# Kernel optimization log

Measured on AMD Instinct MI355X. Metric: run time of the kernel, lower is better.

## Reference

```python
import jax, jax.numpy as jnp
import numpy as np

EPS = 1e-12  # torch F.normalize default eps


def _l2_normalize(t):
    n = jnp.linalg.norm(t, axis=-1, keepdims=True)
    return t / jnp.maximum(n, EPS)


def _block(x, W, alpha):
    # x: [B,H,N,D]; W: [D,D] (torch Linear weight, applied as x @ W.T)
    xn = _l2_normalize(x)                                   # q_norm == k_norm (q=k=x)
    A = jnp.einsum('bhnd,bhmd->bhnm', xn, xn)               # cosine similarity [B,H,N,N]
    A = jax.nn.softmax(A / jnp.maximum(alpha, 0.01), axis=-1)
    av = jnp.einsum('bhnm,bhmd->bhnd', A, x)                # A @ v, v = x
    return jax.nn.relu(jnp.einsum('bhnd,ed->bhne', av, W) + x)


def setup_inputs() -> dict:
    key = jax.random.key(0)
    k1, k2, k3 = jax.random.split(key, 3)
    B, H, N, D = 4, 4, 4096, 64
    x = jax.random.normal(k1, (B, H, N, D), dtype=jnp.float32)
    # nn.Linear(dim, dim, bias=False) weights, kaiming-uniform-ish scale
    bound = 1.0 / np.sqrt(D)
    W1 = jax.random.uniform(k2, (D, D), dtype=jnp.float32, minval=-bound, maxval=bound)
    W2 = jax.random.uniform(k3, (D, D), dtype=jnp.float32, minval=-bound, maxval=bound)
    alpha1 = jnp.float32(1.0)
    alpha2 = jnp.float32(1.0)
    return {"x": x, "W1": W1, "W2": W2, "alpha1": alpha1, "alpha2": alpha2}


def reference(x, W1, W2, alpha1, alpha2):
    x = _block(x, W1, alpha1)
    x = _block(x, W2, alpha2)
    return x
```

## Files before the change

### kernel.cpp

```cpp
#include <hip/hip_runtime.h>

typedef unsigned short u16;
typedef unsigned int   u32;
typedef __bf16 bf16x8 __attribute__((ext_vector_type(8)));
typedef float  f32x4  __attribute__((ext_vector_type(4)));

#define BH    16
#define NSEQ  4096
#define DIM   64
#define BM    128
#define BN    64
#define LDP   72
#define LDPP  68
#define NTH   32
#define QTILES (NSEQ / BM)

#define SMEM_U16   27136
#define SK_OFF     0
#define SV_OFF     9216
#define SP_OFF     18432
#define HBUF       4608
#define WOFF       13824

__device__ __forceinline__ float bf2f(u16 u) {
    union { u32 i; float f; } v; v.i = ((u32)u) << 16; return v.f;
}
__device__ __forceinline__ u16 f2bf(float f) {
    union { float f; u32 i; } v; v.f = f;
    u32 r = v.i + 0x7fffu + ((v.i >> 16) & 1u);
    return (u16)(r >> 16);
}
__device__ __forceinline__ u16 f2bf_fast(float f) {
    union { float f; u32 i; } v; v.f = f;
    return (u16)((v.i + 0x8000u) >> 16);
}
#if __has_builtin(__builtin_amdgcn_exp2f)
__device__ __forceinline__ float exp2_raw(float x) { return __builtin_amdgcn_exp2f(x); }
#else
__device__ __forceinline__ float exp2_raw(float x) {
    float r; asm("v_exp_f32 %0, %1" : "=v"(r) : "v"(x)); return r;
}
#endif

__device__ __forceinline__ void lds_barrier() {
    asm volatile("s_waitcnt lgkmcnt(0)\n\ts_barrier" ::: "memory");
}

__global__ __launch_bounds__(256) void ContentGCN_5059471475267_prep(
    const void* __restrict__ src, int isf,
    u16* __restrict__ xn, u16* __restrict__ xT)
{
    __shared__ u16 tile[256 * 72];
    int bh = blockIdx.x >> 4, nt = blockIdx.x & 15, tid = threadIdx.x;
    size_t base = ((size_t)bh * NSEQ + nt * 256 + tid) * DIM;

    float v[64];
    if (isf) {
        const float4* g = (const float4*)((const float*)src + base);
#pragma unroll
        for (int i = 0; i < 16; i++) {
            float4 t4 = g[i];
            v[4*i] = t4.x; v[4*i+1] = t4.y; v[4*i+2] = t4.z; v[4*i+3] = t4.w;
        }
    } else {
        alignas(16) u16 tmp[64];
        const uint4* g = (const uint4*)((const u16*)src + base);
#pragma unroll
        for (int i = 0; i < 8; i++) ((uint4*)tmp)[i] = g[i];
#pragma unroll
        for (int d = 0; d < 64; d++) v[d] = bf2f(tmp[d]);
    }

    float ss = 0.f;
#pragma unroll
    for (int d = 0; d < 64; d++) ss += v[d] * v[d];
    float n = sqrtf(ss);
    if (n < 1e-12f) n = 1e-12f;
    float inv = 1.0f / n;

    alignas(16) u16 nb[64], rb[64];
#pragma unroll
    for (int d = 0; d < 64; d++) { nb[d] = f2bf(v[d] * inv); rb[d] = f2bf(v[d]); }
    uint4* gn = (uint4*)(xn + base);
#pragma unroll
    for (int i = 0; i < 8; i++) gn[i] = ((uint4*)nb)[i];

    uint4* trow = (uint4*)&tile[tid * 72];
#pragma unroll
    for (int i = 0; i < 8; i++) trow[i] = ((uint4*)rb)[i];
    __syncthreads();

    int d = tid & 63, ch = tid >> 6;
    alignas(16) u16 ob[64];
#pragma unroll
    for (int nn = 0; nn < 64; nn++) ob[nn] = tile[(ch * 64 + nn) * 72 + d];
    uint4* gt = (uint4*)(xT + ((size_t)bh * DIM + d) * NSEQ + (size_t)nt * 256 + ch * 64);
#pragma unroll
    for (int i = 0; i < 8; i++) gt[i] = ((uint4*)ob)[i];
}

__global__ __launch_bounds__(512, 4) void ContentGCN_5059471475267_attn(
    const u16* __restrict__ xn, const u16* __restrict__ xT,
    const void* __restrict__ res, int res_isf,
    const float* __restrict__ Wt, const float* __restrict__ alphap,
    void* __restrict__ outp, int out_isf)
{
    __shared__ u16 smem[SMEM_U16];
    u16* sK = smem + SK_OFF;
    u16* sV = smem + SV_OFF;
    u16* sP = smem + SP_OFF;

    int tid  = threadIdx.x;
    int w    = tid >> 6, lane = tid & 63;
    int half = w >> 2,  wv   = w & 3;
    int quad = lane >> 4, l16 = lane & 15;
    int bh   = blockIdx.x >> 5;
    int qt   = blockIdx.x & 31;

    float scale = 1.4426950408889634f / fmaxf(alphap[0], 0.01f);

    union { u16 s[8]; bf16x8 v; } onesu;
#pragma unroll
    for (int i = 0; i < 8; i++) onesu.s[i] = 0x3F80;
    bf16x8 onesB = onesu.v;

    int qrowA = qt * BM + wv * 16 + l16;
    size_t qbaseA = ((size_t)bh * NSEQ + qrowA) * DIM;
    size_t qbaseB = qbaseA + (size_t)64 * DIM;
    bf16x8 aQ00 = *(const bf16x8*)(xn + qbaseA + quad * 8);
    bf16x8 aQ01 = *(const bf16x8*)(xn + qbaseA + 32 + quad * 8);
    bf16x8 aQ10 = *(const bf16x8*)(xn + qbaseB + quad * 8);
    bf16x8 aQ11 = *(const bf16x8*)(xn + qbaseB + 32 + quad * 8);

    const f32x4 fzero = {0.f, 0.f, 0.f, 0.f};
    f32x4 O0[4], O1[4];
#pragma unroll
    for (int t = 0; t < 4; t++) { O0[t] = fzero; O1[t] = fzero; }
    f32x4 l0 = fzero, l1 = fzero;

    u16* sKh = sK + half * HBUF;
    u16* sVh = sV + half * HBUF;
    u16* sPw = sP + w * (16 * LDPP);

    int ltid = tid & 255;
    int srow = ltid >> 2, scol = (ltid & 3) * 16;

    const u16* pk = xn + ((size_t)bh * NSEQ + half * (NTH * BN) + srow) * DIM + scol;
    const u16* pv = xT + ((size_t)bh * DIM + srow) * NSEQ + half * (NTH * BN) + scol;
    uint4 ck0 = ((const uint4*)pk)[0], ck1 = ((const uint4*)pk)[1];
    uint4 cv0 = ((const uint4*)pv)[0], cv1 = ((const uint4*)pv)[1];
    pk += (size_t)BN * DIM; pv += BN;

    for (int kt = 0; kt < NTH; kt++) {
        lds_barrier();
        *(uint4*)&sKh[srow * LDP + scol]     = ck0;
        *(uint4*)&sKh[srow * LDP + scol + 8] = ck1;
        *(uint4*)&sVh[srow * LDP + scol]     = cv0;
        *(uint4*)&sVh[srow * LDP + scol + 8] = cv1;
        if (kt + 1 < NTH) {
            ck0 = ((const uint4*)pk)[0]; ck1 = ((const uint4*)pk)[1];
            cv0 = ((const uint4*)pv)[0]; cv1 = ((const uint4*)pv)[1];
            pk += (size_t)BN * DIM; pv += BN;
        }
        lds_barrier();

        f32x4 S0[4], S1[4];
#pragma unroll
        for (int t = 0; t < 4; t++) {
            bf16x8 b0 = *(const bf16x8*)&sKh[(l16 + 16 * t) * LDP + quad * 8];
            bf16x8 b1 = *(const bf16x8*)&sKh[(l16 + 16 * t) * LDP + 32 + quad * 8];
            S0[t] = __builtin_amdgcn_mfma_f32_16x16x32_bf16(aQ01, b1,
                    __builtin_amdgcn_mfma_f32_16x16x32_bf16(aQ00, b0, fzero, 0, 0, 0), 0, 0, 0);
            S1[t] = __builtin_amdgcn_mfma_f32_16x16x32_bf16(aQ11, b1,
                    __builtin_amdgcn_mfma_f32_16x16x32_bf16(aQ10, b0, fzero, 0, 0, 0), 0, 0, 0);
        }

        union { uint2 u[2]; bf16x8 v; } pA00, pA01, pA10, pA11;
#pragma unroll
        for (int r = 0; r < 4; r++)
#pragma unroll
            for (int t = 0; t < 4; t++)
                sPw[(quad * 4 + r) * LDPP + l16 + 16 * t] =
                    f2bf_fast(exp2_raw(fmaf(S0[t][r], scale, -scale)));
        pA00.u[0] = *(const uint2*)&sPw[l16 * LDPP + quad * 8];
        pA00.u[1] = *(const uint2*)&sPw[l16 * LDPP + quad * 8 + 4];
        pA01.u[0] = *(const uint2*)&sPw[l16 * LDPP + 32 + quad * 8];
        pA01.u[1] = *(const uint2*)&sPw[l16 * LDPP + 32 + quad * 8 + 4];
        l0 = __builtin_amdgcn_mfma_f32_16x16x32_bf16(pA00.v, onesB, l0, 0, 0, 0);
        l0 = __builtin_amdgcn_mfma_f32_16x16x32_bf16(pA01.v, onesB, l0, 0, 0, 0);

#pragma unroll
        for (int r = 0; r < 4; r++)
#pragma unroll
            for (int t = 0; t < 4; t++)
                sPw[(quad * 4 + r) * LDPP + l16 + 16 * t] =
                    f2bf_fast(exp2_raw(fmaf(S1[t][r], scale, -scale)));
        pA10.u[0] = *(const uint2*)&sPw[l16 * LDPP + quad * 8];
        pA10.u[1] = *(const uint2*)&sPw[l16 * LDPP + quad * 8 + 4];
        pA11.u[0] = *(const uint2*)&sPw[l16 * LDPP + 32 + quad * 8];
        pA11.u[1] = *(const uint2*)&sPw[l16 * LDPP + 32 + quad * 8 + 4];
        l1 = __builtin_amdgcn_mfma_f32_16x16x32_bf16(pA10.v, onesB, l1, 0, 0, 0);
        l1 = __builtin_amdgcn_mfma_f32_16x16x32_bf16(pA11.v, onesB, l1, 0, 0, 0);

#pragma unroll
        for (int t = 0; t < 4; t++) {
            bf16x8 vb0 = *(const bf16x8*)&sVh[(l16 + 16 * t) * LDP + quad * 8];
            bf16x8 vb1 = *(const bf16x8*)&sVh[(l16 + 16 * t) * LDP + 32 + quad * 8];
            O0[t] = __builtin_amdgcn_mfma_f32_16x16x32_bf16(pA01.v, vb1,
                    __builtin_amdgcn_mfma_f32_16x16x32_bf16(pA00.v, vb0, O0[t], 0, 0, 0), 0, 0, 0);
            O1[t] = __builtin_amdgcn_mfma_f32_16x16x32_bf16(pA11.v, vb1,
                    __builtin_amdgcn_mfma_f32_16x16x32_bf16(pA10.v, vb0, O1[t], 0, 0, 0), 0, 0, 0);
        }
    }

    __syncthreads();

    {
        f32x4* Oo = (half == 0) ? O1 : O0;
        f32x4  lo = (half == 0) ? l1 : l0;
        alignas(16) u16 ob[16];
#pragma unroll
        for (int t = 0; t < 4; t++)
#pragma unroll
            for (int r = 0; r < 4; r++) ob[t * 4 + r] = f2bf(Oo[t][r]);
        *(uint4*)&smem[tid * 16]     = ((uint4*)ob)[0];
        *(uint4*)&smem[tid * 16 + 8] = ((uint4*)ob)[1];
        float4* lsc = (float4*)(smem + 8192);
        lsc[tid] = make_float4(lo[0], lo[1], lo[2], lo[3]);
    }
    {
        int r = tid >> 3, c0 = (tid & 7) * 8;
        const float4* gw = (const float4*)(Wt + r * DIM + c0);
        float4 t0 = gw[0], t1 = gw[1];
        alignas(16) u16 wb[8];
        wb[0] = f2bf(t0.x); wb[1] = f2bf(t0.y); wb[2] = f2bf(t0.z); wb[3] = f2bf(t0.w);
        wb[4] = f2bf(t1.x); wb[5] = f2bf(t1.y); wb[6] = f2bf(t1.z); wb[7] = f2bf(t1.w);
        *(uint4*)&smem[WOFF + r * LDP + c0] = *(uint4*)wb;
    }
    __syncthreads();

    f32x4* Om = (half == 0) ? O0 : O1;
    f32x4  lm = (half == 0) ? l0 : l1;
    {
        int partner = tid ^ 256;
        alignas(16) u16 ob[16];
        ((uint4*)ob)[0] = *(const uint4*)&smem[partner * 16];
        ((uint4*)ob)[1] = *(const uint4*)&smem[partner * 16 + 8];
#pragma unroll
        for (int t = 0; t < 4; t++)
#pragma unroll
            for (int r = 0; r < 4; r++) Om[t][r] += bf2f(ob[t * 4 + r]);
        float4 lp = ((const float4*)(smem + 8192))[partner];
        lm[0] += lp.x; lm[1] += lp.y; lm[2] += lp.z; lm[3] += lp.w;
    }

#pragma unroll
    for (int r = 0; r < 4; r++) {
        float invl = 1.0f / lm[r];
#pragma unroll
        for (int t = 0; t < 4; t++)
            sPw[(quad * 4 + r) * LDPP + l16 + 16 * t] = f2bf_fast(Om[t][r] * invl);
    }
    union { uint2 u[2]; bf16x8 v; } aA0, aA1;
    aA0.u[0] = *(const uint2*)&sPw[l16 * LDPP + quad * 8];
    aA0.u[1] = *(const uint2*)&sPw[l16 * LDPP + quad * 8 + 4];
    aA1.u[0] = *(const uint2*)&sPw[l16 * LDPP + 32 + quad * 8];
    aA1.u[1] = *(const uint2*)&sPw[l16 * LDPP + 32 + quad * 8 + 4];

    const u16* sW = smem + WOFF;
    f32x4 R[4];
#pragma unroll
    for (int t = 0; t < 4; t++) {
        bf16x8 b0 = *(const bf16x8*)&sW[(l16 + 16 * t) * LDP + quad * 8];
        bf16x8 b1 = *(const bf16x8*)&sW[(l16 + 16 * t) * LDP + 32 + quad * 8];
        R[t] = __builtin_amdgcn_mfma_f32_16x16x32_bf16(aA1.v, b1,
               __builtin_amdgcn_mfma_f32_16x16x32_bf16(aA0.v, b0, fzero, 0, 0, 0), 0, 0, 0);
    }
#pragma unroll
    for (int t = 0; t < 4; t++) {
#pragma unroll
        for (int r = 0; r < 4; r++) {
            int row = qt * BM + wv * 16 + half * 64 + quad * 4 + r;
            int col = l16 + 16 * t;
            size_t idx = ((size_t)bh * NSEQ + row) * DIM + col;
            float rv = res_isf ? ((const float*)res)[idx] : bf2f(((const u16*)res)[idx]);
            float v = R[t][r] + rv;
            v = (v < 0.f) ? 0.f : v;
            if (out_isf) ((float*)outp)[idx] = v;
            else         ((u16*)outp)[idx]  = f2bf(v);
        }
    }
}

extern "C" void kernel_launch(void* const* d_in, const int* in_sizes, int n_in,
                              void* d_out, int out_size, void* d_ws, size_t ws_size,
                              hipStream_t stream) {
    const float* x  = (const float*)d_in[0];
    const float* W1 = (const float*)d_in[1];
    const float* W2 = (const float*)d_in[2];
    const float* a1 = (const float*)d_in[3];
    const float* a2 = (const float*)d_in[4];
    float* outp = (float*)d_out;

    size_t elems = (size_t)BH * NSEQ * DIM;
    u16* xn = (u16*)d_ws;
    u16* xT = xn + elems;
    u16* y1 = xT + elems;

    dim3 pgrid(BH * 16),     pblk(256);
    dim3 agrid(BH * QTILES), ablk(512);

    ContentGCN_5059471475267_prep<<<pgrid, pblk, 0, stream>>>(x, 1, xn, xT);
    ContentGCN_5059471475267_attn<<<agrid, ablk, 0, stream>>>(xn, xT, x, 1, W1, a1, y1, 0);
    ContentGCN_5059471475267_prep<<<pgrid, pblk, 0, stream>>>(y1, 0, xn, xT);
    ContentGCN_5059471475267_attn<<<agrid, ablk, 0, stream>>>(xn, xT, y1, 0, W2, a2, outp, 1);
}
```

Baseline: 283.0 us.

## Switch attention to 32x32 MFMA with register-resident P via permlane swaps

Rewrites the attention inner loop to compute transposed score tiles with 32x32x16 bf16 MFMA. The probabilities are packed to bf16 and rearranged in registers with v_cvt_pk_bf16_f32 and v_permlane32_swap, which removes the LDS round-trip for P. Row sums now come from VALU adds instead of ones-matrix MFMAs. The output projection is applied per half and the two halves are summed in fp32 LDS, replacing the bf16 partner exchange, and the final stores are coalesced. The prep kernel is split into smaller blocks with a shuffle-based norm reduction. The main risks are register pressure from the f32x16 accumulators and reliance on gfx950-specific instructions.

```diff
diff --git a/kernel.cpp b/kernel.cpp
--- a/kernel.cpp
+++ b/kernel.cpp
@@ -3,7 +3,7 @@
 typedef unsigned short u16;
 typedef unsigned int   u32;
 typedef __bf16 bf16x8 __attribute__((ext_vector_type(8)));
-typedef float  f32x4  __attribute__((ext_vector_type(4)));
+typedef float  f32x16 __attribute__((ext_vector_type(16)));
 
 #define BH    16
 #define NSEQ  4096
@@ -11,16 +11,15 @@
 #define BM    128
 #define BN    64
 #define LDP   72
-#define LDPP  68
 #define NTH   32
 #define QTILES (NSEQ / BM)
 
-#define SMEM_U16   27136
-#define SK_OFF     0
-#define SV_OFF     9216
-#define SP_OFF     18432
-#define HBUF       4608
-#define WOFF       13824
+#define SK_OFF   0
+#define SV_OFF   9216
+#define SW_OFF   18432
+#define LX_OFF   23040
+#define SMEM_U16 23552
+#define HBUF     4608
 
 __device__ __forceinline__ float bf2f(u16 u) {
     union { u32 i; float f; } v; v.i = ((u32)u) << 16; return v.f;
@@ -29,10 +28,6 @@
     union { float f; u32 i; } v; v.f = f;
     u32 r = v.i + 0x7fffu + ((v.i >> 16) & 1u);
     return (u16)(r >> 16);
-}
-__device__ __forceinline__ u16 f2bf_fast(float f) {
-    union { float f; u32 i; } v; v.f = f;
-    return (u16)((v.i + 0x8000u) >> 16);
 }
 #if __has_builtin(__builtin_amdgcn_exp2f)
 __device__ __forceinline__ float exp2_raw(float x) { return __builtin_amdgcn_exp2f(x); }
@@ -41,7 +36,12 @@
     float r; asm("v_exp_f32 %0, %1" : "=v"(r) : "v"(x)); return r;
 }
 #endif
-
+__device__ __forceinline__ u32 cvtpk(float a, float b) {
+    u32 r; asm("v_cvt_pk_bf16_f32 %0, %1, %2" : "=v"(r) : "v"(a), "v"(b)); return r;
+}
+__device__ __forceinline__ void plswap(u32& a, u32& b) {
+    asm("v_permlane32_swap_b32 %0, %1" : "+v"(a), "+v"(b));
+}
 __device__ __forceinline__ void lds_barrier() {
     asm volatile("s_waitcnt lgkmcnt(0)\n\ts_barrier" ::: "memory");
 }
@@ -50,53 +50,52 @@
     const void* __restrict__ src, int isf,
     u16* __restrict__ xn, u16* __restrict__ xT)
 {
-    __shared__ u16 tile[256 * 72];
-    int bh = blockIdx.x >> 4, nt = blockIdx.x & 15, tid = threadIdx.x;
-    size_t base = ((size_t)bh * NSEQ + nt * 256 + tid) * DIM;
-
-    float v[64];
+    __shared__ u16 tile[64 * 72];
+    int bh = blockIdx.x >> 6, nt = blockIdx.x & 63, tid = threadIdx.x;
+    int r = tid >> 2, cg = (tid & 3) * 16;
+    size_t base = ((size_t)bh * NSEQ + nt * 64 + r) * DIM + cg;
+
+    float v[16];
     if (isf) {
         const float4* g = (const float4*)((const float*)src + base);
 #pragma unroll
-        for (int i = 0; i < 16; i++) {
-            float4 t4 = g[i];
-            v[4*i] = t4.x; v[4*i+1] = t4.y; v[4*i+2] = t4.z; v[4*i+3] = t4.w;
+        for (int i = 0; i < 4; i++) {
+            float4 t = g[i];
+            v[4*i] = t.x; v[4*i+1] = t.y; v[4*i+2] = t.z; v[4*i+3] = t.w;
         }
     } else {
-        alignas(16) u16 tmp[64];
+        alignas(16) u16 tmp[16];
         const uint4* g = (const uint4*)((const u16*)src + base);
-#pragma unroll
-        for (int i = 0; i < 8; i++) ((uint4*)tmp)[i] = g[i];
-#pragma unroll
-        for (int d = 0; d < 64; d++) v[d] = bf2f(tmp[d]);
+        ((uint4*)tmp)[0] = g[0]; ((uint4*)tmp)[1] = g[1];
+#pragma unroll
+        for (int d = 0; d < 16; d++) v[d] = bf2f(tmp[d]);
     }
 
     float ss = 0.f;
 #pragma unroll
-    for (int d = 0; d < 64; d++) ss += v[d] * v[d];
+    for (int d = 0; d < 16; d++) ss += v[d] * v[d];
+    ss += __shfl_xor(ss, 1);
+    ss += __shfl_xor(ss, 2);
     float n = sqrtf(ss);
     if (n < 1e-12f) n = 1e-12f;
     float inv = 1.0f / n;
 
-    alignas(16) u16 nb[64], rb[64];
-#pragma unroll
-    for (int d = 0; d < 64; d++) { nb[d] = f2bf(v[d] * inv); rb[d] = f2bf(v[d]); }
+    alignas(16) u16 nb[16], rb[16];
+#pragma unroll
+    for (int d = 0; d < 16; d++) { nb[d] = f2bf(v[d] * inv); rb[d] = f2bf(v[d]); }
     uint4* gn = (uint4*)(xn + base);
-#pragma unroll
-    for (int i = 0; i < 8; i++) gn[i] = ((uint4*)nb)[i];
-
-    uint4* trow = (uint4*)&tile[tid * 72];
-#pragma unroll
-    for (int i = 0; i < 8; i++) trow[i] = ((uint4*)rb)[i];
-    __syncthreads();
-
-    int d = tid & 63, ch = tid >> 6;
-    alignas(16) u16 ob[64];
-#pragma unroll
-    for (int nn = 0; nn < 64; nn++) ob[nn] = tile[(ch * 64 + nn) * 72 + d];
-    uint4* gt = (uint4*)(xT + ((size_t)bh * DIM + d) * NSEQ + (size_t)nt * 256 + ch * 64);
-#pragma unroll
-    for (int i = 0; i < 8; i++) gt[i] = ((uint4*)ob)[i];
+    gn[0] = ((uint4*)nb)[0]; gn[1] = ((uint4*)nb)[1];
+
+    uint4* tr = (uint4*)&tile[r * 72 + cg];
+    tr[0] = ((uint4*)rb)[0]; tr[1] = ((uint4*)rb)[1];
+    __syncthreads();
+
+    int d = tid >> 2, sc = (tid & 3) * 16;
+    alignas(16) u16 ob[16];
+#pragma unroll
+    for (int j = 0; j < 16; j++) ob[j] = tile[(sc + j) * 72 + d];
+    uint4* gt = (uint4*)(xT + ((size_t)bh * DIM + d) * NSEQ + (size_t)nt * 64 + sc);
+    gt[0] = ((uint4*)ob)[0]; gt[1] = ((uint4*)ob)[1];
 }
 
 __global__ __launch_bounds__(512, 4) void ContentGCN_5059471475267_attn(
@@ -108,39 +107,43 @@
     __shared__ u16 smem[SMEM_U16];
     u16* sK = smem + SK_OFF;
     u16* sV = smem + SV_OFF;
-    u16* sP = smem + SP_OFF;
+    u16* sW = smem + SW_OFF;
+    float* lX = (float*)(smem + LX_OFF);
 
     int tid  = threadIdx.x;
     int w    = tid >> 6, lane = tid & 63;
     int half = w >> 2,  wv   = w & 3;
-    int quad = lane >> 4, l16 = lane & 15;
+    int l31  = lane & 31, hi = lane >> 5;
     int bh   = blockIdx.x >> 5;
     int qt   = blockIdx.x & 31;
 
     float scale = 1.4426950408889634f / fmaxf(alphap[0], 0.01f);
 
-    union { u16 s[8]; bf16x8 v; } onesu;
-#pragma unroll
-    for (int i = 0; i < 8; i++) onesu.s[i] = 0x3F80;
-    bf16x8 onesB = onesu.v;
-
-    int qrowA = qt * BM + wv * 16 + l16;
-    size_t qbaseA = ((size_t)bh * NSEQ + qrowA) * DIM;
-    size_t qbaseB = qbaseA + (size_t)64 * DIM;
-    bf16x8 aQ00 = *(const bf16x8*)(xn + qbaseA + quad * 8);
-    bf16x8 aQ01 = *(const bf16x8*)(xn + qbaseA + 32 + quad * 8);
-    bf16x8 aQ10 = *(const bf16x8*)(xn + qbaseB + quad * 8);
-    bf16x8 aQ11 = *(const bf16x8*)(xn + qbaseB + 32 + quad * 8);
-
-    const f32x4 fzero = {0.f, 0.f, 0.f, 0.f};
-    f32x4 O0[4], O1[4];
-#pragma unroll
-    for (int t = 0; t < 4; t++) { O0[t] = fzero; O1[t] = fzero; }
-    f32x4 l0 = fzero, l1 = fzero;
+    {
+        int rr = tid >> 3, c0 = (tid & 7) * 8;
+        const float4* gw = (const float4*)(Wt + rr * DIM + c0);
+        float4 t0 = gw[0], t1 = gw[1];
+        alignas(16) u16 wb[8];
+        wb[0] = f2bf(t0.x); wb[1] = f2bf(t0.y); wb[2] = f2bf(t0.z); wb[3] = f2bf(t0.w);
+        wb[4] = f2bf(t1.x); wb[5] = f2bf(t1.y); wb[6] = f2bf(t1.z); wb[7] = f2bf(t1.w);
+        *(uint4*)&sW[rr * LDP + c0] = *(const uint4*)wb;
+    }
+
+    int qrow = qt * BM + wv * 32 + l31;
+    const u16* qp = xn + ((size_t)bh * NSEQ + qrow) * DIM + hi * 8;
+    bf16x8 bQ0 = *(const bf16x8*)(qp);
+    bf16x8 bQ1 = *(const bf16x8*)(qp + 16);
+    bf16x8 bQ2 = *(const bf16x8*)(qp + 32);
+    bf16x8 bQ3 = *(const bf16x8*)(qp + 48);
+
+    f32x16 z16;
+#pragma unroll
+    for (int i = 0; i < 16; i++) z16[i] = 0.f;
+    f32x16 OT0 = z16, OT1 = z16;
+    float la0 = 0.f, la1 = 0.f, la2 = 0.f, la3 = 0.f;
 
     u16* sKh = sK + half * HBUF;
     u16* sVh = sV + half * HBUF;
-    u16* sPw = sP + w * (16 * LDPP);
 
     int ltid = tid & 255;
     int srow = ltid >> 2, scol = (ltid & 3) * 16;
@@ -150,6 +153,10 @@
     uint4 ck0 = ((const uint4*)pk)[0], ck1 = ((const uint4*)pk)[1];
     uint4 cv0 = ((const uint4*)pv)[0], cv1 = ((const uint4*)pv)[1];
     pk += (size_t)BN * DIM; pv += BN;
+
+    const u16* kB = sKh + l31 * LDP + hi * 8;
+    const u16* vB0 = sVh + l31 * LDP + hi * 8;
+    const u16* vB1 = sVh + (32 + l31) * LDP + hi * 8;
 
     for (int kt = 0; kt < NTH; kt++) {
         lds_barrier();
@@ -164,130 +171,151 @@
         }
         lds_barrier();
 
-        f32x4 S0[4], S1[4];
-#pragma unroll
-        for (int t = 0; t < 4; t++) {
-            bf16x8 b0 = *(const bf16x8*)&sKh[(l16 + 16 * t) * LDP + quad * 8];
-            bf16x8 b1 = *(const bf16x8*)&sKh[(l16 + 16 * t) * LDP + 32 + quad * 8];
-            S0[t] = __builtin_amdgcn_mfma_f32_16x16x32_bf16(aQ01, b1,
-                    __builtin_amdgcn_mfma_f32_16x16x32_bf16(aQ00, b0, fzero, 0, 0, 0), 0, 0, 0);
-            S1[t] = __builtin_amdgcn_mfma_f32_16x16x32_bf16(aQ11, b1,
-                    __builtin_amdgcn_mfma_f32_16x16x32_bf16(aQ10, b0, fzero, 0, 0, 0), 0, 0, 0);
-        }
-
-        union { uint2 u[2]; bf16x8 v; } pA00, pA01, pA10, pA11;
-#pragma unroll
-        for (int r = 0; r < 4; r++)
-#pragma unroll
-            for (int t = 0; t < 4; t++)
-                sPw[(quad * 4 + r) * LDPP + l16 + 16 * t] =
-                    f2bf_fast(exp2_raw(fmaf(S0[t][r], scale, -scale)));
-        pA00.u[0] = *(const uint2*)&sPw[l16 * LDPP + quad * 8];
-        pA00.u[1] = *(const uint2*)&sPw[l16 * LDPP + quad * 8 + 4];
-        pA01.u[0] = *(const uint2*)&sPw[l16 * LDPP + 32 + quad * 8];
-        pA01.u[1] = *(const uint2*)&sPw[l16 * LDPP + 32 + quad * 8 + 4];
-        l0 = __builtin_amdgcn_mfma_f32_16x16x32_bf16(pA00.v, onesB, l0, 0, 0, 0);
-        l0 = __builtin_amdgcn_mfma_f32_16x16x32_bf16(pA01.v, onesB, l0, 0, 0, 0);
-
-#pragma unroll
-        for (int r = 0; r < 4; r++)
-#pragma unroll
-            for (int t = 0; t < 4; t++)
-                sPw[(quad * 4 + r) * LDPP + l16 + 16 * t] =
-                    f2bf_fast(exp2_raw(fmaf(S1[t][r], scale, -scale)));
-        pA10.u[0] = *(const uint2*)&sPw[l16 * LDPP + quad * 8];
-        pA10.u[1] = *(const uint2*)&sPw[l16 * LDPP + quad * 8 + 4];
-        pA11.u[0] = *(const uint2*)&sPw[l16 * LDPP + 32 + quad * 8];
-        pA11.u[1] = *(const uint2*)&sPw[l16 * LDPP + 32 + quad * 8 + 4];
-        l1 = __builtin_amdgcn_mfma_f32_16x16x32_bf16(pA10.v, onesB, l1, 0, 0, 0);
-        l1 = __builtin_amdgcn_mfma_f32_16x16x32_bf16(pA11.v, onesB, l1, 0, 0, 0);
-
-#pragma unroll
-        for (int t = 0; t < 4; t++) {
-            bf16x8 vb0 = *(const bf16x8*)&sVh[(l16 + 16 * t) * LDP + quad * 8];
-            bf16x8 vb1 = *(const bf16x8*)&sVh[(l16 + 16 * t) * LDP + 32 + quad * 8];
-            O0[t] = __builtin_amdgcn_mfma_f32_16x16x32_bf16(pA01.v, vb1,
-                    __builtin_amdgcn_mfma_f32_16x16x32_bf16(pA00.v, vb0, O0[t], 0, 0, 0), 0, 0, 0);
-            O1[t] = __builtin_amdgcn_mfma_f32_16x16x32_bf16(pA11.v, vb1,
-                    __builtin_amdgcn_mfma_f32_16x16x32_bf16(pA10.v, vb0, O1[t], 0, 0, 0), 0, 0, 0);
-        }
-    }
-
-    __syncthreads();
-
+#pragma unroll
+        for (int kb = 0; kb < 2; kb++) {
+            const u16* kb0 = kB + kb * 32 * LDP;
+            f32x16 ST;
+            ST = __builtin_amdgcn_mfma_f32_32x32x16_bf16(*(const bf16x8*)(kb0),      bQ0, z16, 0, 0, 0);
+            ST = __builtin_amdgcn_mfma_f32_32x32x16_bf16(*(const bf16x8*)(kb0 + 16), bQ1, ST,  0, 0, 0);
+            ST = __builtin_amdgcn_mfma_f32_32x32x16_bf16(*(const bf16x8*)(kb0 + 32), bQ2, ST,  0, 0, 0);
+            ST = __builtin_amdgcn_mfma_f32_32x32x16_bf16(*(const bf16x8*)(kb0 + 48), bQ3, ST,  0, 0, 0);
+
+            float p0  = exp2_raw(fmaf(ST[0],  scale, -scale));
+            float p1  = exp2_raw(fmaf(ST[1],  scale, -scale));
+            float p2  = exp2_raw(fmaf(ST[2],  scale, -scale));
+            float p3  = exp2_raw(fmaf(ST[3],  scale, -scale));
+            float p4  = exp2_raw(fmaf(ST[4],  scale, -scale));
+            float p5  = exp2_raw(fmaf(ST[5],  scale, -scale));
+            float p6  = exp2_raw(fmaf(ST[6],  scale, -scale));
+            float p7  = exp2_raw(fmaf(ST[7],  scale, -scale));
+            float p8  = exp2_raw(fmaf(ST[8],  scale, -scale));
+            float p9  = exp2_raw(fmaf(ST[9],  scale, -scale));
+            float p10 = exp2_raw(fmaf(ST[10], scale, -scale));
+            float p11 = exp2_raw(fmaf(ST[11], scale, -scale));
+            float p12 = exp2_raw(fmaf(ST[12], scale, -scale));
+            float p13 = exp2_raw(fmaf(ST[13], scale, -scale));
+            float p14 = exp2_raw(fmaf(ST[14], scale, -scale));
+            float p15 = exp2_raw(fmaf(ST[15], scale, -scale));
+
+            la0 += (p0 + p4) + (p8  + p12);
+            la1 += (p1 + p5) + (p9  + p13);
+            la2 += (p2 + p6) + (p10 + p14);
+            la3 += (p3 + p7) + (p11 + p15);
+
+            u32 w0 = cvtpk(p0,  p1),  w1 = cvtpk(p2,  p3);
+            u32 w2 = cvtpk(p4,  p5),  w3 = cvtpk(p6,  p7);
+            u32 w4 = cvtpk(p8,  p9),  w5 = cvtpk(p10, p11);
+            u32 w6 = cvtpk(p12, p13), w7 = cvtpk(p14, p15);
+            plswap(w0, w2); plswap(w1, w3);
+            plswap(w4, w6); plswap(w5, w7);
+            union { u32 u[4]; bf16x8 v; } bp0, bp1;
+            bp0.u[0] = w0; bp0.u[1] = w1; bp0.u[2] = w2; bp0.u[3] = w3;
+            bp1.u[0] = w4; bp1.u[1] = w5; bp1.u[2] = w6; bp1.u[3] = w7;
+
+            const u16* v0 = vB0 + kb * 32;
+            const u16* v1 = vB1 + kb * 32;
+            OT0 = __builtin_amdgcn_mfma_f32_32x32x16_bf16(*(const bf16x8*)(v0),      bp0.v, OT0, 0, 0, 0);
+            OT0 = __builtin_amdgcn_mfma_f32_32x32x16_bf16(*(const bf16x8*)(v0 + 16), bp1.v, OT0, 0, 0, 0);
+            OT1 = __builtin_amdgcn_mfma_f32_32x32x16_bf16(*(const bf16x8*)(v1),      bp0.v, OT1, 0, 0, 0);
+            OT1 = __builtin_amdgcn_mfma_f32_32x32x16_bf16(*(const bf16x8*)(v1 + 16), bp1.v, OT1, 0, 0, 0);
+        }
+    }
+
+    float lsum = (la0 + la1) + (la2 + la3);
+    u32 ja = __float_as_uint(lsum), jb = ja;
+    plswap(ja, jb);
+    float lfull = __uint_as_float(ja) + __uint_as_float(jb);
+
+    __syncthreads();
+    if (lane < 32) lX[w * 32 + l31] = lfull;
+    __syncthreads();
+    float invl = 1.0f / (lfull + lX[(w ^ 4) * 32 + l31]);
+
+    union { u32 u[4]; bf16x8 v; } av0, av1, av2, av3;
     {
-        f32x4* Oo = (half == 0) ? O1 : O0;
-        f32x4  lo = (half == 0) ? l1 : l0;
-        alignas(16) u16 ob[16];
-#pragma unroll
-        for (int t = 0; t < 4; t++)
-#pragma unroll
-            for (int r = 0; r < 4; r++) ob[t * 4 + r] = f2bf(Oo[t][r]);
-        *(uint4*)&smem[tid * 16]     = ((uint4*)ob)[0];
-        *(uint4*)&smem[tid * 16 + 8] = ((uint4*)ob)[1];
-        float4* lsc = (float4*)(smem + 8192);
-        lsc[tid] = make_float4(lo[0], lo[1], lo[2], lo[3]);
-    }
+        u32 x0 = cvtpk(OT0[0]  * invl, OT0[1]  * invl), x1 = cvtpk(OT0[2]  * invl, OT0[3]  * invl);
+        u32 x2 = cvtpk(OT0[4]  * invl, OT0[5]  * invl), x3 = cvtpk(OT0[6]  * invl, OT0[7]  * invl);
+        u32 x4 = cvtpk(OT0[8]  * invl, OT0[9]  * invl), x5 = cvtpk(OT0[10] * invl, OT0[11] * invl);
+        u32 x6 = cvtpk(OT0[12] * invl, OT0[13] * invl), x7 = cvtpk(OT0[14] * invl, OT0[15] * invl);
+        plswap(x0, x2); plswap(x1, x3); plswap(x4, x6); plswap(x5, x7);
+        av0.u[0] = x0; av0.u[1] = x1; av0.u[2] = x2; av0.u[3] = x3;
+        av1.u[0] = x4; av1.u[1] = x5; av1.u[2] = x6; av1.u[3] = x7;
+        u32 y0 = cvtpk(OT1[0]  * invl, OT1[1]  * invl), y1 = cvtpk(OT1[2]  * invl, OT1[3]  * invl);
+        u32 y2 = cvtpk(OT1[4]  * invl, OT1[5]  * invl), y3 = cvtpk(OT1[6]  * invl, OT1[7]  * invl);
+        u32 y4 = cvtpk(OT1[8]  * invl, OT1[9]  * invl), y5 = cvtpk(OT1[10] * invl, OT1[11] * invl);
+        u32 y6 = cvtpk(OT1[12] * invl, OT1[13] * invl), y7 = cvtpk(OT1[14] * invl, OT1[15] * invl);
+        plswap(y0, y2); plswap(y1, y3); plswap(y4, y6); plswap(y5, y7);
+        av2.u[0] = y0; av2.u[1] = y1; av2.u[2] = y2; av2.u[3] = y3;
+        av3.u[0] = y4; av3.u[1] = y5; av3.u[2] = y6; av3.u[3] = y7;
+    }
+
+    f32x16 R0, R1;
     {
-        int r = tid >> 3, c0 = (tid & 7) * 8;
-        const float4* gw = (const float4*)(Wt + r * DIM + c0);
-        float4 t0 = gw[0], t1 = gw[1];
-        alignas(16) u16 wb[8];
-        wb[0] = f2bf(t0.x); wb[1] = f2bf(t0.y); wb[2] = f2bf(t0.z); wb[3] = f2bf(t0.w);
-        wb[4] = f2bf(t1.x); wb[5] = f2bf(t1.y); wb[6] = f2bf(t1.z); wb[7] = f2bf(t1.w);
-        *(uint4*)&smem[WOFF + r * LDP + c0] = *(uint4*)wb;
-    }
-    __syncthreads();
-
-    f32x4* Om = (half == 0) ? O0 : O1;
-    f32x4  lm = (half == 0) ? l0 : l1;
+        const u16* w0p = sW + l31 * LDP + hi * 8;
+        const u16* w1p = sW + (32 + l31) * LDP + hi * 8;
+        R0 = __builtin_amdgcn_mfma_f32_32x32x16_bf16(*(const bf16x8*)(w0p),      av0.v, z16, 0, 0, 0);
+        R0 = __builtin_amdgcn_mfma_f32_32x32x16_bf16(*(const bf16x8*)(w0p + 16), av1.v, R0,  0, 0, 0);
+        R0 = __builtin_amdgcn_mfma_f32_32x32x16_bf16(*(const bf16x8*)(w0p + 32), av2.v, R0,  0, 0, 0);
+        R0 = __builtin_amdgcn_mfma_f32_32x32x16_bf16(*(const bf16x8*)(w0p + 48), av3.v, R0,  0, 0, 0);
+        R1 = __builtin_amdgcn_mfma_f32_32x32x16_bf16(*(const bf16x8*)(w1p),      av0.v, z16, 0, 0, 0);
+        R1 = __builtin_amdgcn_mfma_f32_32x32x16_bf16(*(const bf16x8*)(w1p + 16), av1.v, R1,  0, 0, 0);
+        R1 = __builtin_amdgcn_mfma_f32_32x32x16_bf16(*(const bf16x8*)(w1p + 32), av2.v, R1,  0, 0, 0);
+        R1 = __builtin_amdgcn_mfma_f32_32x32x16_bf16(*(const bf16x8*)(w1p + 48), av3.v, R1,  0, 0, 0);
+    }
+
+    float* outS = (float*)smem;
+    if (half == 0) {
+#pragma unroll
+        for (int r = 0; r < 16; r++) {
+            int e0 = (r & 3) + 8 * (r >> 2) + 4 * hi;
+            outS[e0 * 133 + wv * 32 + l31]        = R0[r];
+            outS[(e0 + 32) * 133 + wv * 32 + l31] = R1[r];
+        }
+    }
+    __syncthreads();
+    if (half == 1) {
+#pragma unroll
+        for (int r = 0; r < 16; r++) {
+            int e0 = (r & 3) + 8 * (r >> 2) + 4 * hi;
+            outS[e0 * 133 + wv * 32 + l31]        += R0[r];
+            outS[(e0 + 32) * 133 + wv * 32 + l31] += R1[r];
+        }
+    }
+    __syncthreads();
+
     {
-        int partner = tid ^ 256;
-        alignas(16) u16 ob[16];
-        ((uint4*)ob)[0] = *(const uint4*)&smem[partner * 16];
-        ((uint4*)ob)[1] = *(const uint4*)&smem[partner * 16 + 8];
-#pragma unroll
-        for (int t = 0; t < 4; t++)
-#pragma unroll
-            for (int r = 0; r < 4; r++) Om[t][r] += bf2f(ob[t * 4 + r]);
-        float4 lp = ((const float4*)(smem + 8192))[partner];
-        lm[0] += lp.x; lm[1] += lp.y; lm[2] += lp.z; lm[3] += lp.w;
-    }
-
-#pragma unroll
-    for (int r = 0; r < 4; r++) {
-        float invl = 1.0f / lm[r];
-#pragma unroll
-        for (int t = 0; t < 4; t++)
-            sPw[(quad * 4 + r) * LDPP + l16 + 16 * t] = f2bf_fast(Om[t][r] * invl);
-    }
-    union { uint2 u[2]; bf16x8 v; } aA0, aA1;
-    aA0.u[0] = *(const uint2*)&sPw[l16 * LDPP + quad * 8];
-    aA0.u[1] = *(const uint2*)&sPw[l16 * LDPP + quad * 8 + 4];
-    aA1.u[0] = *(const uint2*)&sPw[l16 * LDPP + 32 + quad * 8];
-    aA1.u[1] = *(const uint2*)&sPw[l16 * LDPP + 32 + quad * 8 + 4];
-
-    const u16* sW = smem + WOFF;
-    f32x4 R[4];
-#pragma unroll
-    for (int t = 0; t < 4; t++) {
-        bf16x8 b0 = *(const bf16x8*)&sW[(l16 + 16 * t) * LDP + quad * 8];
-        bf16x8 b1 = *(const bf16x8*)&sW[(l16 + 16 * t) * LDP + 32 + quad * 8];
-        R[t] = __builtin_amdgcn_mfma_f32_16x16x32_bf16(aA1.v, b1,
-               __builtin_amdgcn_mfma_f32_16x16x32_bf16(aA0.v, b0, fzero, 0, 0, 0), 0, 0, 0);
-    }
-#pragma unroll
-    for (int t = 0; t < 4; t++) {
-#pragma unroll
-        for (int r = 0; r < 4; r++) {
-            int row = qt * BM + wv * 16 + half * 64 + quad * 4 + r;
-            int col = l16 + 16 * t;
-            size_t idx = ((size_t)bh * NSEQ + row) * DIM + col;
-            float rv = res_isf ? ((const float*)res)[idx] : bf2f(((const u16*)res)[idx]);
-            float v = R[t][r] + rv;
-            v = (v < 0.f) ? 0.f : v;
-            if (out_isf) ((float*)outp)[idx] = v;
-            else         ((u16*)outp)[idx]  = f2bf(v);
+        int q = tid >> 2, c = tid & 3;
+        size_t gbase = ((size_t)bh * NSEQ + qt * BM + q) * DIM + c * 16;
+        float vv[16];
+#pragma unroll
+        for (int j = 0; j < 16; j++) vv[j] = outS[(c * 16 + j) * 133 + q];
+        if (res_isf) {
+            const float4* rp = (const float4*)((const float*)res + gbase);
+#pragma unroll
+            for (int i = 0; i < 4; i++) {
+                float4 t = rp[i];
+                vv[4*i] += t.x; vv[4*i+1] += t.y; vv[4*i+2] += t.z; vv[4*i+3] += t.w;
+            }
+        } else {
+            alignas(16) u16 rb[16];
+            const uint4* rp = (const uint4*)((const u16*)res + gbase);
+            ((uint4*)rb)[0] = rp[0]; ((uint4*)rb)[1] = rp[1];
+#pragma unroll
+            for (int j = 0; j < 16; j++) vv[j] += bf2f(rb[j]);
+        }
+#pragma unroll
+        for (int j = 0; j < 16; j++) vv[j] = (vv[j] < 0.f) ? 0.f : vv[j];
+        if (out_isf) {
+            float4* op = (float4*)((float*)outp + gbase);
+#pragma unroll
+            for (int i = 0; i < 4; i++)
+                op[i] = make_float4(vv[4*i], vv[4*i+1], vv[4*i+2], vv[4*i+3]);
+        } else {
+            alignas(16) u16 ob[16];
+#pragma unroll
+            for (int j = 0; j < 16; j++) ob[j] = f2bf(vv[j]);
+            uint4* op = (uint4*)((u16*)outp + gbase);
+            op[0] = ((uint4*)ob)[0]; op[1] = ((uint4*)ob)[1];
         }
     }
 }
@@ -307,7 +335,7 @@
     u16* xT = xn + elems;
     u16* y1 = xT + elems;
 
-    dim3 pgrid(BH * 16),     pblk(256);
+    dim3 pgrid(BH * 64),     pblk(256);
     dim3 agrid(BH * QTILES), ablk(512);
 
     ContentGCN_5059471475267_prep<<<pgrid, pblk, 0, stream>>>(x, 1, xn, xT);
```

After: 248.0 us. 12.4% less time.
